# Kernel optimization log

Hardware: AMD Instinct MI355X
Metric: run time of the kernel (lower is better)

Reference implementation:

```python
import jax, jax.numpy as jnp
import numpy as np

B, L, E, D = 4, 1024, 128, 256
NPOI, EPOI, NH, FF = 10000, 128, 8, 256
HD = D // NH


def layer_norm(x, g, b, eps=1e-5):
    m = x.mean(-1, keepdims=True)
    v = ((x - m) ** 2).mean(-1, keepdims=True)
    return (x - m) / jnp.sqrt(v + eps) * g + b


def leaky_relu(x):
    return jnp.where(x >= 0, x, 0.01 * x)


def tokenize_timestamp(t):
    # t: (..., 2) = [timestamp_sec, delta_sec] -> (..., 4) = [week, hour, minute, d_minute]
    week = t[..., 0] % 604800.0 / 86400.0
    hour = t[..., 0] % 86400.0 / 3600.0
    minute = t[..., 0] % 3600.0 / 60.0
    return jnp.stack([week, hour, minute, t[..., 1] / 60.0], -1)


def pos_encode(pos, d):
    # standard sinusoidal PE evaluated at integer positions `pos`
    freq = jnp.exp(-jnp.log(10000.0) * (2.0 * jnp.arange(d // 2, dtype=jnp.float32)) / d)
    ang = pos[..., None].astype(jnp.float32) * freq  # (..., d/2)
    pe = jnp.zeros(pos.shape + (d,), jnp.float32)
    return pe.at[..., 0::2].set(jnp.sin(ang)).at[..., 1::2].set(jnp.cos(ang))


def setup_inputs():
    ks = iter(jax.random.split(jax.random.key(0), 48))

    def nrm(shape, s=0.02):
        return jax.random.normal(next(ks), shape, jnp.float32) * s

    spatial = jax.random.normal(next(ks), (B, L, 2), jnp.float32) * 10.0
    ts = jax.random.uniform(next(ks), (B, L), jnp.float32, 0.0, 1e6)
    dt = jax.random.uniform(next(ks), (B, L), jnp.float32, 0.0, 3600.0)
    token = jax.random.randint(next(ks), (B, L, 2), 0, 2).astype(jnp.float32)
    iq = jnp.zeros((B, L, 4, 2), jnp.float32)
    iq = iq.at[..., 0, 0].set(spatial[..., 0]).at[..., 1, 0].set(spatial[..., 1])
    iq = iq.at[..., 2, 0].set(ts).at[..., 3, 0].set(dt)
    iq = iq.at[..., 0, 1].set(token[..., 0]).at[..., 2, 1].set(token[..., 1])
    positions = jax.random.randint(next(ks), (B, L, 2), 0, L)
    return dict(
        input_seq=iq, positions=positions,
        poi_coors=jax.random.normal(next(ks), (NPOI, 2), jnp.float32) * 10.0,
        poi_embed_mat=nrm((NPOI, EPOI), 1.0),
        sp_w1=nrm((2, E)), sp_b1=jnp.zeros((E,), jnp.float32),
        sp_w2=nrm((E, D)), sp_b2=jnp.zeros((D,), jnp.float32),
        four_w=nrm((4, E), 1.0), four_b=nrm((4, E), 1.0),
        te_w=nrm((4 * E, D)), te_b=jnp.zeros((D,), jnp.float32),
        poi_ln_g=jnp.ones((EPOI,), jnp.float32), poi_ln_b=jnp.zeros((EPOI,), jnp.float32),
        poi_w=nrm((EPOI, D)), poi_b=jnp.zeros((D,), jnp.float32),
        tok_emb=nrm((6, E), 1.0).at[5].set(0.0),
        tok_ln_g=jnp.ones((E,), jnp.float32), tok_ln_b=jnp.zeros((E,), jnp.float32),
        tok_w=nrm((E, D)), tok_b=jnp.zeros((D,), jnp.float32),
        mha_in_w=nrm((D, 3 * D)), mha_in_b=jnp.zeros((3 * D,), jnp.float32),
        mha_out_w=nrm((D, D)), mha_out_b=jnp.zeros((D,), jnp.float32),
        ln1_g=jnp.ones((D,), jnp.float32), ln1_b=jnp.zeros((D,), jnp.float32),
        ff_w1=nrm((D, FF)), ff_b1=jnp.zeros((FF,), jnp.float32),
        ff_w2=nrm((FF, D)), ff_b2=jnp.zeros((D,), jnp.float32),
        ln2_g=jnp.ones((D,), jnp.float32), ln2_b=jnp.zeros((D,), jnp.float32))


def reference(input_seq, positions, poi_coors, poi_embed_mat,
              sp_w1, sp_b1, sp_w2, sp_b2, four_w, four_b, te_w, te_b,
              poi_ln_g, poi_ln_b, poi_w, poi_b,
              tok_emb, tok_ln_g, tok_ln_b, tok_w, tok_b,
              mha_in_w, mha_in_b, mha_out_w, mha_out_b,
              ln1_g, ln1_b, ff_w1, ff_b1, ff_w2, ff_b2, ln2_g, ln2_b):
    token = input_seq[..., jnp.array([0, 2]), 1].astype(jnp.int32)  # (B,L,2)
    spatial = input_seq[:, :, 0:2, 0]                                # (B,L,2)
    tt = tokenize_timestamp(input_seq[:, :, 2:4, 0])                 # (B,L,4)
    # token embedding: Embedding(6) -> LN -> Linear -> (B,L,2,D)
    tok_e = layer_norm(tok_emb[token], tok_ln_g, tok_ln_b) @ tok_w + tok_b
    # spatial embedding (note: original's masked_fill is non-inplace and discarded)
    sp_e = leaky_relu(spatial @ sp_w1 + sp_b1) @ sp_w2 + sp_b2 + tok_e[:, :, 0]
    # brute-force nearest POI: cdist^2 + argmin + gather
    d2 = ((poi_coors[None, None] - spatial[:, :, None]) ** 2).sum(-1)  # (B,L,NPOI)
    poi = jnp.argmin(d2, -1)                                           # (B,L)
    poi_e = layer_norm(poi_embed_mat[poi], poi_ln_g, poi_ln_b) @ poi_w + poi_b + tok_e[:, :, 0]
    # temporal: 4 FourierEncode modules -> concat -> LeakyReLU -> Linear
    t_e = jnp.cos(tt[..., None] * four_w + four_b).reshape(B, L, 4 * E)
    t_e = leaky_relu(t_e) @ te_w + te_b + tok_e[:, :, 1]
    # modal mixer: 1-layer post-norm TransformerEncoder over the 3 modalities
    x = jnp.stack([sp_e, t_e, poi_e], 2).reshape(B * L, 3, D)
    qkv = x @ mha_in_w + mha_in_b
    q, k, v = jnp.split(qkv, 3, -1)
    q = q.reshape(B * L, 3, NH, HD)
    k = k.reshape(B * L, 3, NH, HD)
    v = v.reshape(B * L, 3, NH, HD)
    att = jax.nn.softmax(jnp.einsum('nqhd,nkhd->nhqk', q, k) / jnp.sqrt(jnp.float32(HD)), -1)
    o = jnp.einsum('nhqk,nkhd->nqhd', att, v).reshape(B * L, 3, D) @ mha_out_w + mha_out_b
    x = layer_norm(x + o, ln1_g, ln1_b)
    x = layer_norm(x + (jax.nn.relu(x @ ff_w1 + ff_b1) @ ff_w2 + ff_b2), ln2_g, ln2_b)
    modal_h = x.reshape(B, L, 3, D).mean(2)
    modal_h = modal_h + pos_encode(positions[..., 0], D) + pos_encode(positions[..., 1], D)
    return modal_h  # == mem_seq in the original forward
```

## Files before the change

kernel.cpp:

```cpp
#include <hip/hip_runtime.h>
#include <math.h>

namespace {
constexpr int E = 128, D = 256;
constexpr int NPOI = 10000, NH = 8, FFD = 256;
constexpr int HD = D / NH;
constexpr int NTOK = 4096;
constexpr int TA = 8;
constexpr int TB = 4;
constexpr float LN_EPS = 1e-5f;

constexpr int PK_QKV = 0;
constexpr int PK_OUT = 196608;
constexpr int PK_FF1 = 262144;
constexpr int PK_FF2 = 327680;
constexpr int PK_E0  = 393216;
constexpr int PK_E1  = 458752;
constexpr int PK_E2  = 622592;
constexpr int PK_TOTAL = 688128;
constexpr int NTILES = PK_TOTAL / 512;
}

using frag8 = __attribute__((ext_vector_type(8))) short;
using f32x4 = __attribute__((ext_vector_type(4))) float;

__device__ __forceinline__ float bf2f(short s) {
    union { unsigned u; float f; } x; x.u = ((unsigned)(unsigned short)s) << 16; return x.f;
}
__device__ __forceinline__ unsigned short f2bf(float f) {
    union { float f; unsigned u; } x; x.f = f;
    unsigned r = x.u + 0x7fffu + ((x.u >> 16) & 1u);
    return (unsigned short)(r >> 16);
}

__device__ __forceinline__ float wsum64(float v) {
#pragma unroll
    for (int m = 1; m < 64; m <<= 1) v += __shfl_xor(v, m);
    return v;
}

__device__ __forceinline__ void ln128_bf(const float* __restrict__ src,
                                         const float* __restrict__ g,
                                         const float* __restrict__ b,
                                         short* __restrict__ dst1,
                                         short* __restrict__ dst2, int lane) {
    float v0 = src[lane], v1 = src[64 + lane];
    float mean = wsum64(v0 + v1) * (1.0f / 128.0f);
    float d0 = v0 - mean, d1 = v1 - mean;
    float var = wsum64(d0 * d0 + d1 * d1) * (1.0f / 128.0f);
    float inv = sqrtf(var + LN_EPS);
    float y0 = d0 / inv * g[lane] + b[lane];
    float y1 = d1 / inv * g[64 + lane] + b[64 + lane];
    unsigned short s0 = f2bf(y0), s1 = f2bf(y1);
    dst1[lane] = (short)s0; dst1[64 + lane] = (short)s1;
    if (dst2) { dst2[lane] = (short)s0; dst2[64 + lane] = (short)s1; }
}

__global__ __launch_bounds__(256)
void pack_weights(const float* __restrict__ wqkv, const float* __restrict__ wout,
                  const float* __restrict__ fw1,  const float* __restrict__ fw2,
                  const float* __restrict__ sp_w2, const float* __restrict__ te_w,
                  const float* __restrict__ poi_w, const float* __restrict__ tok_w,
                  unsigned short* __restrict__ pk)
{
    __shared__ float buf[4][32 * 17];
    const int wv = threadIdx.x >> 6, lane = threadIdx.x & 63;
    const int tile = blockIdx.x * 4 + wv;
    if (tile >= NTILES) return;

    int t = tile, sel, base;
    if (t < 384)              { sel = 0; base = PK_QKV; }
    else if ((t -= 384) < 128){ sel = 1; base = PK_OUT; }
    else if ((t -= 128) < 128){ sel = 2; base = PK_FF1; }
    else if ((t -= 128) < 128){ sel = 3; base = PK_FF2; }
    else if ((t -= 128) < 128){ sel = 4; base = PK_E0; }
    else if ((t -= 128) < 320){ sel = 5; base = PK_E1; }
    else                      { t -= 320; sel = 6; base = PK_E2; }
    const int NKT = (sel == 5) ? 20 : 8;
    const int nt = t / NKT, kt = t % NKT;

    const int k = kt * 32 + (lane >> 1);
    const int n0 = nt * 16 + (lane & 1) * 8;
    const float* row;
    switch (sel) {
        case 0:  row = wqkv + (size_t)k * 768; break;
        case 1:  row = wout + (size_t)k * 256; break;
        case 2:  row = fw1  + (size_t)k * 256; break;
        case 3:  row = fw2  + (size_t)k * 256; break;
        case 4:  row = (k < 128) ? sp_w2 + (size_t)k * 256 : tok_w + (size_t)(k - 128) * 256; break;
        case 5:  row = (k < 512) ? te_w  + (size_t)k * 256 : tok_w + (size_t)(k - 512) * 256; break;
        default: row = (k < 128) ? poi_w + (size_t)k * 256 : tok_w + (size_t)(k - 128) * 256; break;
    }
    float4 v0 = *(const float4*)(row + n0);
    float4 v1 = *(const float4*)(row + n0 + 4);
    float* b = buf[wv];
    const int wb = (lane >> 1) * 17 + (lane & 1) * 8;
    b[wb + 0] = v0.x; b[wb + 1] = v0.y; b[wb + 2] = v0.z; b[wb + 3] = v0.w;
    b[wb + 4] = v1.x; b[wb + 5] = v1.y; b[wb + 6] = v1.z; b[wb + 7] = v1.w;
    __syncthreads();

    const int rb = (lane >> 4) * 8, c = lane & 15;
    frag8 fr;
#pragma unroll
    for (int j = 0; j < 8; ++j) fr[j] = (short)f2bf(b[(rb + j) * 17 + c]);
    *(frag8*)(pk + base + ((size_t)t * 64 + lane) * 8) = fr;
}

__global__ __launch_bounds__(256, 2)
void embed_mfma(const float* __restrict__ iq,
                const float* __restrict__ poi_coors,
                const float* __restrict__ poi_embed,
                const float* __restrict__ sp_w1, const float* __restrict__ sp_b1,
                const float* __restrict__ sp_b2,
                const float* __restrict__ four_w, const float* __restrict__ four_b,
                const float* __restrict__ te_b,
                const float* __restrict__ poi_ln_g, const float* __restrict__ poi_ln_b,
                const float* __restrict__ poi_b,
                const float* __restrict__ tok_emb,
                const float* __restrict__ tok_ln_g, const float* __restrict__ tok_ln_b,
                const float* __restrict__ tok_b,
                const unsigned short* __restrict__ pk,
                unsigned short* __restrict__ xout)
{
    constexpr int P0 = 264, P1 = 648, P2 = 264;
    const int tid = threadIdx.x;
    const int w = tid >> 6, lane = tid & 63;
    const int quad = lane >> 4, l16 = lane & 15;
    const int n0 = blockIdx.x * TA;

    __shared__ __align__(16) short U[12544];
    __shared__ __align__(16) short s_x[TA * 768];
    __shared__ float s_meta[TA][6];
    __shared__ int   s_tok[TA][2];
    __shared__ float s_wd[4][TA];
    __shared__ int   s_wi[4][TA];
    __shared__ int   s_poi[TA];

    short* h0 = U;
    short* h1 = U + 2112;
    short* h2 = U + 7296;

    if (tid < TA) {
        const float* p = iq + (size_t)(n0 + tid) * 8;
        s_meta[tid][0] = p[0];
        s_meta[tid][1] = p[2];
        float ts = p[4];
        float dt = p[6];
        s_tok[tid][0] = (int)p[1];
        s_tok[tid][1] = (int)p[5];
        s_meta[tid][2] = fmodf(ts, 604800.0f) / 86400.0f;
        s_meta[tid][3] = fmodf(ts, 86400.0f) / 3600.0f;
        s_meta[tid][4] = fmodf(ts, 3600.0f) / 60.0f;
        s_meta[tid][5] = dt / 60.0f;
    }
    __syncthreads();

    {
        float sx[TA], sy[TA], bd[TA];
        int bi[TA];
#pragma unroll
        for (int t = 0; t < TA; ++t) {
            sx[t] = s_meta[t][0]; sy[t] = s_meta[t][1];
            bd[t] = INFINITY; bi[t] = NPOI;
        }
        const float2* pc = (const float2*)poi_coors;
        for (int i = tid; i < NPOI; i += 256) {
            float2 p = pc[i];
#pragma unroll
            for (int t = 0; t < TA; ++t) {
                float dx = __fsub_rn(p.x, sx[t]);
                float dy = __fsub_rn(p.y, sy[t]);
                float d  = __fadd_rn(__fmul_rn(dx, dx), __fmul_rn(dy, dy));
                if (d < bd[t]) { bd[t] = d; bi[t] = i; }
            }
        }
#pragma unroll
        for (int m = 1; m < 64; m <<= 1) {
#pragma unroll
            for (int t = 0; t < TA; ++t) {
                float od = __shfl_xor(bd[t], m);
                int   oi = __shfl_xor(bi[t], m);
                if (od < bd[t] || (od == bd[t] && oi < bi[t])) { bd[t] = od; bi[t] = oi; }
            }
        }
        if (lane == 0) {
#pragma unroll
            for (int t = 0; t < TA; ++t) { s_wd[w][t] = bd[t]; s_wi[w][t] = bi[t]; }
        }
        __syncthreads();
        if (tid < TA) {
            float bdd = s_wd[0][tid]; int bii = s_wi[0][tid];
#pragma unroll
            for (int ww = 1; ww < 4; ++ww) {
                float od = s_wd[ww][tid]; int oi = s_wi[ww][tid];
                if (od < bdd || (od == bdd && oi < bii)) { bdd = od; bii = oi; }
            }
            s_poi[tid] = bii;
        }
        __syncthreads();
    }

#pragma unroll
    for (int k2 = 0; k2 < 2; ++k2) {
        const int t = w + k2 * 4;
        ln128_bf(tok_emb + (size_t)s_tok[t][0] * E, tok_ln_g, tok_ln_b,
                 h0 + t * P0 + 128, h2 + t * P2 + 128, lane);
        ln128_bf(tok_emb + (size_t)s_tok[t][1] * E, tok_ln_g, tok_ln_b,
                 h1 + t * P1 + 512, nullptr, lane);
        ln128_bf(poi_embed + (size_t)s_poi[t] * E, poi_ln_g, poi_ln_b,
                 h2 + t * P2, nullptr, lane);
    }

    for (int idx = tid; idx < TA * 128; idx += 256) {
        int t = idx >> 7, l = idx & 127;
        float h = s_meta[t][0] * sp_w1[l] + s_meta[t][1] * sp_w1[128 + l] + sp_b1[l];
        h0[t * P0 + l] = (short)f2bf((h >= 0.0f) ? h : 0.01f * h);
    }
    for (int idx = tid; idx < TA * 512; idx += 256) {
        int t = idx >> 9, jj = idx & 511, f = jj >> 7;
        float c = cosf(s_meta[t][2 + f] * four_w[jj] + four_b[jj]);
        h1[t * P1 + jj] = (short)f2bf((c >= 0.0f) ? c : 0.01f * c);
    }
    __syncthreads();

    {
        f32x4 acc[4];
#pragma unroll
        for (int nt = 0; nt < 4; ++nt) {
            int c = w * 64 + nt * 16 + l16;
            float bv = sp_b2[c] + tok_b[c];
            acc[nt][0] = bv; acc[nt][1] = bv; acc[nt][2] = bv; acc[nt][3] = bv;
        }
        for (int kt = 0; kt < 8; ++kt) {
            frag8 a = *(const frag8*)(&h0[l16 * P0 + kt * 32 + quad * 8]);
#pragma unroll
            for (int nt = 0; nt < 4; ++nt) {
                frag8 b = *(const frag8*)(pk + PK_E0 + (((size_t)(w * 4 + nt) * 8 + kt) * 64 + lane) * 8);
                acc[nt] = __builtin_amdgcn_mfma_f32_16x16x32_bf16(a, b, acc[nt], 0, 0, 0);
            }
        }
        if (quad < 2) {
#pragma unroll
            for (int nt = 0; nt < 4; ++nt)
#pragma unroll
                for (int r = 0; r < 4; ++r)
                    s_x[(quad * 4 + r) * 768 + w * 64 + nt * 16 + l16] = (short)f2bf(acc[nt][r]);
        }
    }
    {
        f32x4 acc[4];
#pragma unroll
        for (int nt = 0; nt < 4; ++nt) {
            int c = w * 64 + nt * 16 + l16;
            float bv = te_b[c] + tok_b[c];
            acc[nt][0] = bv; acc[nt][1] = bv; acc[nt][2] = bv; acc[nt][3] = bv;
        }
        for (int kt = 0; kt < 20; ++kt) {
            frag8 a = *(const frag8*)(&h1[l16 * P1 + kt * 32 + quad * 8]);
#pragma unroll
            for (int nt = 0; nt < 4; ++nt) {
                frag8 b = *(const frag8*)(pk + PK_E1 + (((size_t)(w * 4 + nt) * 20 + kt) * 64 + lane) * 8);
                acc[nt] = __builtin_amdgcn_mfma_f32_16x16x32_bf16(a, b, acc[nt], 0, 0, 0);
            }
        }
        if (quad < 2) {
#pragma unroll
            for (int nt = 0; nt < 4; ++nt)
#pragma unroll
                for (int r = 0; r < 4; ++r)
                    s_x[(quad * 4 + r) * 768 + 256 + w * 64 + nt * 16 + l16] = (short)f2bf(acc[nt][r]);
        }
    }
    {
        f32x4 acc[4];
#pragma unroll
        for (int nt = 0; nt < 4; ++nt) {
            int c = w * 64 + nt * 16 + l16;
            float bv = poi_b[c] + tok_b[c];
            acc[nt][0] = bv; acc[nt][1] = bv; acc[nt][2] = bv; acc[nt][3] = bv;
        }
        for (int kt = 0; kt < 8; ++kt) {
            frag8 a = *(const frag8*)(&h2[l16 * P2 + kt * 32 + quad * 8]);
#pragma unroll
            for (int nt = 0; nt < 4; ++nt) {
                frag8 b = *(const frag8*)(pk + PK_E2 + (((size_t)(w * 4 + nt) * 8 + kt) * 64 + lane) * 8);
                acc[nt] = __builtin_amdgcn_mfma_f32_16x16x32_bf16(a, b, acc[nt], 0, 0, 0);
            }
        }
        if (quad < 2) {
#pragma unroll
            for (int nt = 0; nt < 4; ++nt)
#pragma unroll
                for (int r = 0; r < 4; ++r)
                    s_x[(quad * 4 + r) * 768 + 512 + w * 64 + nt * 16 + l16] = (short)f2bf(acc[nt][r]);
        }
    }
    __syncthreads();

    {
        unsigned short* xg = xout + (size_t)n0 * 768;
        for (int c = tid; c < TA * 96; c += 256)
            *(frag8*)(xg + c * 8) = *(const frag8*)(&s_x[c * 8]);
    }
}

__global__ __launch_bounds__(256, 3)
void mha_ff_mfma(const unsigned short* __restrict__ xin,
                 const unsigned short* __restrict__ pk,
                 const float* __restrict__ bqkv, const float* __restrict__ bout,
                 const float* __restrict__ ln1g, const float* __restrict__ ln1b,
                 const float* __restrict__ fb1,  const float* __restrict__ fb2,
                 const float* __restrict__ ln2g, const float* __restrict__ ln2b,
                 const int* __restrict__ positions,
                 float* __restrict__ out)
{
    constexpr int PA = 264;
    constexpr int PQ = 776;
    constexpr int PF = 260;
    const int tid = threadIdx.x;
    const int w = tid >> 6, lane = tid & 63;
    const int quad = lane >> 4, l16 = lane & 15;
    const int n0tok = blockIdx.x * TB;
    const unsigned short* xg = xin + (size_t)n0tok * 3 * D;

    __shared__ __align__(16) short s_a[16 * PA];
    __shared__ __align__(16) char  Uq[25088];
    __shared__ float s_att[TB * NH * 9];

    short* qkv = (short*)Uq;
    float* s_f = (float*)Uq;
    short* s_h = (short*)(Uq + 16640);

    for (int i = tid; i < 12 * 32; i += 256) {
        int row = i >> 5, col = (i & 31) * 8;
        *(frag8*)(&s_a[row * PA + col]) = *(const frag8*)(xg + row * 256 + col);
    }
    __syncthreads();

    float xres[16];

    {
        f32x4 acc[12];
#pragma unroll
        for (int nt = 0; nt < 12; ++nt) {
            float bv = bqkv[w * 192 + nt * 16 + l16];
            acc[nt][0] = bv; acc[nt][1] = bv; acc[nt][2] = bv; acc[nt][3] = bv;
        }
        for (int kt = 0; kt < 8; ++kt) {
            frag8 a = *(const frag8*)(&s_a[l16 * PA + kt * 32 + quad * 8]);
#pragma unroll
            for (int nt = 0; nt < 12; ++nt) {
                frag8 b = *(const frag8*)(pk + PK_QKV + (((size_t)(w * 12 + nt) * 8 + kt) * 64 + lane) * 8);
                acc[nt] = __builtin_amdgcn_mfma_f32_16x16x32_bf16(a, b, acc[nt], 0, 0, 0);
            }
        }
#pragma unroll
        for (int nt = 0; nt < 4; ++nt)
#pragma unroll
            for (int r = 0; r < 4; ++r)
                xres[nt * 4 + r] = bf2f(s_a[(quad * 4 + r) * PA + w * 64 + nt * 16 + l16]);
#pragma unroll
        for (int nt = 0; nt < 12; ++nt)
#pragma unroll
            for (int r = 0; r < 4; ++r) {
                int row = quad * 4 + r, col = w * 192 + nt * 16 + l16;
                qkv[row * PQ + col] = (short)f2bf(acc[nt][r]);
            }
    }
    __syncthreads();

    for (int idx3 = tid; idx3 < TB * NH * 3; idx3 += 256) {
        int tok = idx3 / 24, rem = idx3 % 24;
        int h = rem / 3, qr = rem % 3;
        const short* qp = qkv + (tok * 3 + qr) * PQ + h * HD;
        const short* k0 = qkv + (tok * 3 + 0) * PQ + D + h * HD;
        const short* k1 = qkv + (tok * 3 + 1) * PQ + D + h * HD;
        const short* k2 = qkv + (tok * 3 + 2) * PQ + D + h * HD;
        float s0 = 0.0f, s1 = 0.0f, s2 = 0.0f;
#pragma unroll
        for (int u = 0; u < HD; ++u) {
            float q = bf2f(qp[u]);
            s0 += q * bf2f(k0[u]);
            s1 += q * bf2f(k1[u]);
            s2 += q * bf2f(k2[u]);
        }
        const float sc = 1.0f / sqrtf((float)HD);
        s0 *= sc; s1 *= sc; s2 *= sc;
        float m = fmaxf(s0, fmaxf(s1, s2));
        float e0 = expf(s0 - m), e1 = expf(s1 - m), e2 = expf(s2 - m);
        float inv = 1.0f / (e0 + e1 + e2);
        s_att[idx3 * 3 + 0] = e0 * inv;
        s_att[idx3 * 3 + 1] = e1 * inv;
        s_att[idx3 * 3 + 2] = e2 * inv;
    }
    __syncthreads();

    {
        const int h = tid >> 5;
#pragma unroll
        for (int tok = 0; tok < TB; ++tok) {
            float v0 = bf2f(qkv[(tok * 3 + 0) * PQ + 2 * D + tid]);
            float v1 = bf2f(qkv[(tok * 3 + 1) * PQ + 2 * D + tid]);
            float v2 = bf2f(qkv[(tok * 3 + 2) * PQ + 2 * D + tid]);
#pragma unroll
            for (int qr = 0; qr < 3; ++qr) {
                const float* a = s_att + tok * 72 + h * 9 + qr * 3;
                s_a[(tok * 3 + qr) * PA + tid] = (short)f2bf(a[0] * v0 + a[1] * v1 + a[2] * v2);
            }
        }
    }
    __syncthreads();

    {
        f32x4 acc[4];
#pragma unroll
        for (int nt = 0; nt < 4; ++nt) {
            float bv = bout[w * 64 + nt * 16 + l16];
            acc[nt][0] = bv; acc[nt][1] = bv; acc[nt][2] = bv; acc[nt][3] = bv;
        }
        for (int kt = 0; kt < 8; ++kt) {
            frag8 a = *(const frag8*)(&s_a[l16 * PA + kt * 32 + quad * 8]);
#pragma unroll
            for (int nt = 0; nt < 4; ++nt) {
                frag8 b = *(const frag8*)(pk + PK_OUT + (((size_t)(w * 4 + nt) * 8 + kt) * 64 + lane) * 8);
                acc[nt] = __builtin_amdgcn_mfma_f32_16x16x32_bf16(a, b, acc[nt], 0, 0, 0);
            }
        }
        __syncthreads();
#pragma unroll
        for (int nt = 0; nt < 4; ++nt)
#pragma unroll
            for (int r = 0; r < 4; ++r) {
                int row = quad * 4 + r, col = w * 64 + nt * 16 + l16;
                s_f[row * PF + col] = acc[nt][r] + xres[nt * 4 + r];
            }
    }
    __syncthreads();

#pragma unroll
    for (int rr = 0; rr < 4; ++rr) {
        int row = w + rr * 4, col = lane * 4;
        float4 v = *(const float4*)(&s_f[row * PF + col]);
        float mean = wsum64(v.x + v.y + v.z + v.w) * (1.0f / 256.0f);
        float dx = v.x - mean, dy = v.y - mean, dz = v.z - mean, dw = v.w - mean;
        float var = wsum64(dx * dx + dy * dy + dz * dz + dw * dw) * (1.0f / 256.0f);
        float s = sqrtf(var + LN_EPS);
        float4 g = *(const float4*)(ln1g + col), b = *(const float4*)(ln1b + col);
        float y0 = dx / s * g.x + b.x, y1 = dy / s * g.y + b.y;
        float y2 = dz / s * g.z + b.z, y3 = dw / s * g.w + b.w;
        float4 yv; yv.x = y0; yv.y = y1; yv.z = y2; yv.w = y3;
        *(float4*)(&s_f[row * PF + col]) = yv;
        ushort4 bb; bb.x = f2bf(y0); bb.y = f2bf(y1); bb.z = f2bf(y2); bb.w = f2bf(y3);
        *(ushort4*)(&s_a[row * PA + col]) = bb;
    }
    __syncthreads();

    {
        f32x4 acc[4];
#pragma unroll
        for (int nt = 0; nt < 4; ++nt) {
            float bv = fb1[w * 64 + nt * 16 + l16];
            acc[nt][0] = bv; acc[nt][1] = bv; acc[nt][2] = bv; acc[nt][3] = bv;
        }
        for (int kt = 0; kt < 8; ++kt) {
            frag8 a = *(const frag8*)(&s_a[l16 * PA + kt * 32 + quad * 8]);
#pragma unroll
            for (int nt = 0; nt < 4; ++nt) {
                frag8 b = *(const frag8*)(pk + PK_FF1 + (((size_t)(w * 4 + nt) * 8 + kt) * 64 + lane) * 8);
                acc[nt] = __builtin_amdgcn_mfma_f32_16x16x32_bf16(a, b, acc[nt], 0, 0, 0);
            }
        }
#pragma unroll
        for (int nt = 0; nt < 4; ++nt)
#pragma unroll
            for (int r = 0; r < 4; ++r) {
                int row = quad * 4 + r, col = w * 64 + nt * 16 + l16;
                s_h[row * PA + col] = (short)f2bf(fmaxf(acc[nt][r], 0.0f));
            }
    }
    __syncthreads();

    {
        f32x4 acc[4];
#pragma unroll
        for (int nt = 0; nt < 4; ++nt) {
            float bv = fb2[w * 64 + nt * 16 + l16];
            acc[nt][0] = bv; acc[nt][1] = bv; acc[nt][2] = bv; acc[nt][3] = bv;
        }
        for (int kt = 0; kt < 8; ++kt) {
            frag8 a = *(const frag8*)(&s_h[l16 * PA + kt * 32 + quad * 8]);
#pragma unroll
            for (int nt = 0; nt < 4; ++nt) {
                frag8 b = *(const frag8*)(pk + PK_FF2 + (((size_t)(w * 4 + nt) * 8 + kt) * 64 + lane) * 8);
                acc[nt] = __builtin_amdgcn_mfma_f32_16x16x32_bf16(a, b, acc[nt], 0, 0, 0);
            }
        }
#pragma unroll
        for (int nt = 0; nt < 4; ++nt)
#pragma unroll
            for (int r = 0; r < 4; ++r) {
                int row = quad * 4 + r, col = w * 64 + nt * 16 + l16;
                float y = s_f[row * PF + col];
                s_f[row * PF + col] = acc[nt][r] + y;
            }
    }
    __syncthreads();

#pragma unroll
    for (int rr = 0; rr < 4; ++rr) {
        int row = w + rr * 4, col = lane * 4;
        float4 v = *(const float4*)(&s_f[row * PF + col]);
        float mean = wsum64(v.x + v.y + v.z + v.w) * (1.0f / 256.0f);
        float dx = v.x - mean, dy = v.y - mean, dz = v.z - mean, dw = v.w - mean;
        float var = wsum64(dx * dx + dy * dy + dz * dz + dw * dw) * (1.0f / 256.0f);
        float s = sqrtf(var + LN_EPS);
        float4 g = *(const float4*)(ln2g + col), b = *(const float4*)(ln2b + col);
        float4 zv;
        zv.x = dx / s * g.x + b.x; zv.y = dy / s * g.y + b.y;
        zv.z = dz / s * g.z + b.z; zv.w = dw / s * g.w + b.w;
        *(float4*)(&s_f[row * PF + col]) = zv;
    }
    __syncthreads();

    {
        const int fi = tid >> 1;
        const float freq = expf(-logf(10000.0f) * (2.0f * fi) / (float)D);
#pragma unroll
        for (int t = 0; t < TB; ++t) {
            int n = n0tok + t;
            float m3 = (s_f[(3 * t) * PF + tid] + s_f[(3 * t + 1) * PF + tid] +
                        s_f[(3 * t + 2) * PF + tid]) / 3.0f;
            float p0 = (float)positions[2 * n], p1 = (float)positions[2 * n + 1];
            float a0 = p0 * freq, a1 = p1 * freq;
            float pe = (tid & 1) ? (cosf(a0) + cosf(a1)) : (sinf(a0) + sinf(a1));
            out[(size_t)n * D + tid] = m3 + pe;
        }
    }
}

extern "C" void kernel_launch(void* const* d_in, const int* in_sizes, int n_in,
                              void* d_out, int out_size, void* d_ws, size_t ws_size,
                              hipStream_t stream)
{
    const float* iq        = (const float*)d_in[0];
    const int*   positions = (const int*)d_in[1];
    const float* poi_coors = (const float*)d_in[2];
    const float* poi_embed = (const float*)d_in[3];
    const float* sp_w1     = (const float*)d_in[4];
    const float* sp_b1     = (const float*)d_in[5];
    const float* sp_w2     = (const float*)d_in[6];
    const float* sp_b2     = (const float*)d_in[7];
    const float* four_w    = (const float*)d_in[8];
    const float* four_b    = (const float*)d_in[9];
    const float* te_w      = (const float*)d_in[10];
    const float* te_b      = (const float*)d_in[11];
    const float* poi_ln_g  = (const float*)d_in[12];
    const float* poi_ln_b  = (const float*)d_in[13];
    const float* poi_w     = (const float*)d_in[14];
    const float* poi_b     = (const float*)d_in[15];
    const float* tok_emb   = (const float*)d_in[16];
    const float* tok_ln_g  = (const float*)d_in[17];
    const float* tok_ln_b  = (const float*)d_in[18];
    const float* tok_w     = (const float*)d_in[19];
    const float* tok_b     = (const float*)d_in[20];
    const float* mha_in_w  = (const float*)d_in[21];
    const float* mha_in_b  = (const float*)d_in[22];
    const float* mha_out_w = (const float*)d_in[23];
    const float* mha_out_b = (const float*)d_in[24];
    const float* ln1_g     = (const float*)d_in[25];
    const float* ln1_b     = (const float*)d_in[26];
    const float* ff_w1     = (const float*)d_in[27];
    const float* ff_b1     = (const float*)d_in[28];
    const float* ff_w2     = (const float*)d_in[29];
    const float* ff_b2     = (const float*)d_in[30];
    const float* ln2_g     = (const float*)d_in[31];
    const float* ln2_b     = (const float*)d_in[32];

    unsigned short* pkw = (unsigned short*)d_ws;
    unsigned short* xws = (unsigned short*)((char*)d_ws + PK_TOTAL * 2);

    pack_weights<<<NTILES / 4, 256, 0, stream>>>(
        mha_in_w, mha_out_w, ff_w1, ff_w2, sp_w2, te_w, poi_w, tok_w, pkw);

    embed_mfma<<<NTOK / TA, 256, 0, stream>>>(
        iq, poi_coors, poi_embed, sp_w1, sp_b1, sp_b2, four_w, four_b, te_b,
        poi_ln_g, poi_ln_b, poi_b, tok_emb, tok_ln_g, tok_ln_b, tok_b,
        pkw, xws);

    mha_ff_mfma<<<NTOK / TB, 256, 0, stream>>>(
        xws, pkw, mha_in_b, mha_out_b, ln1_g, ln1_b,
        ff_b1, ff_b2, ln2_g, ln2_b, positions, (float*)d_out);
}
```

Before: 204.8 us.

## Process eight tokens per block in MHA/FF kernel to reuse weight fragments

Doubles the tokens handled per block in the fused MHA+FFN kernel from 4 to 8, giving 24 rows, which are computed as two 16-row MFMA tiles sharing each loaded weight fragment. This halves global weight traffic per token and halves the block count. In exchange it uses more registers and LDS, lowers the launch-bounds occupancy hint from 3 to 2, and leaves 8 of the 32 MFMA rows as padding. The remaining unshown sections (attention loop, positional encoding, output) must also handle TB=8 correctly.

```diff
diff --git a/kernel.cpp b/kernel.cpp
--- a/kernel.cpp
+++ b/kernel.cpp
@@ -7,7 +7,7 @@
 constexpr int HD = D / NH;
 constexpr int NTOK = 4096;
 constexpr int TA = 8;
-constexpr int TB = 4;
+constexpr int TB = 8;
 constexpr float LN_EPS = 1e-5f;
 
 constexpr int PK_QKV = 0;
@@ -304,7 +304,7 @@
     }
 }
 
-__global__ __launch_bounds__(256, 3)
+__global__ __launch_bounds__(256, 2)
 void mha_ff_mfma(const unsigned short* __restrict__ xin,
                  const unsigned short* __restrict__ pk,
                  const float* __restrict__ bqkv, const float* __restrict__ bout,
@@ -317,54 +317,68 @@
     constexpr int PA = 264;
     constexpr int PQ = 776;
     constexpr int PF = 260;
+    constexpr int NROW = 3 * TB;
     const int tid = threadIdx.x;
     const int w = tid >> 6, lane = tid & 63;
     const int quad = lane >> 4, l16 = lane & 15;
     const int n0tok = blockIdx.x * TB;
     const unsigned short* xg = xin + (size_t)n0tok * 3 * D;
 
-    __shared__ __align__(16) short s_a[16 * PA];
-    __shared__ __align__(16) char  Uq[25088];
+    __shared__ __align__(16) short s_a[32 * PA];
+    __shared__ __align__(16) char  Uq[41856];
     __shared__ float s_att[TB * NH * 9];
 
     short* qkv = (short*)Uq;
     float* s_f = (float*)Uq;
-    short* s_h = (short*)(Uq + 16640);
-
-    for (int i = tid; i < 12 * 32; i += 256) {
+    short* s_h = (short*)(Uq + 24960);
+
+    for (int i = tid; i < NROW * 32; i += 256) {
         int row = i >> 5, col = (i & 31) * 8;
         *(frag8*)(&s_a[row * PA + col]) = *(const frag8*)(xg + row * 256 + col);
     }
     __syncthreads();
 
-    float xres[16];
-
-    {
-        f32x4 acc[12];
+    float xres[32];
+
+    {
+        f32x4 acc[24];
 #pragma unroll
         for (int nt = 0; nt < 12; ++nt) {
             float bv = bqkv[w * 192 + nt * 16 + l16];
-            acc[nt][0] = bv; acc[nt][1] = bv; acc[nt][2] = bv; acc[nt][3] = bv;
+#pragma unroll
+            for (int m = 0; m < 2; ++m) {
+                acc[nt * 2 + m][0] = bv; acc[nt * 2 + m][1] = bv;
+                acc[nt * 2 + m][2] = bv; acc[nt * 2 + m][3] = bv;
+            }
         }
         for (int kt = 0; kt < 8; ++kt) {
-            frag8 a = *(const frag8*)(&s_a[l16 * PA + kt * 32 + quad * 8]);
+            frag8 a0 = *(const frag8*)(&s_a[l16 * PA + kt * 32 + quad * 8]);
+            frag8 a1 = *(const frag8*)(&s_a[(16 + l16) * PA + kt * 32 + quad * 8]);
 #pragma unroll
             for (int nt = 0; nt < 12; ++nt) {
                 frag8 b = *(const frag8*)(pk + PK_QKV + (((size_t)(w * 12 + nt) * 8 + kt) * 64 + lane) * 8);
-                acc[nt] = __builtin_amdgcn_mfma_f32_16x16x32_bf16(a, b, acc[nt], 0, 0, 0);
-            }
-        }
-#pragma unroll
-        for (int nt = 0; nt < 4; ++nt)
-#pragma unroll
-            for (int r = 0; r < 4; ++r)
-                xres[nt * 4 + r] = bf2f(s_a[(quad * 4 + r) * PA + w * 64 + nt * 16 + l16]);
+                acc[nt * 2 + 0] = __builtin_amdgcn_mfma_f32_16x16x32_bf16(a0, b, acc[nt * 2 + 0], 0, 0, 0);
+                acc[nt * 2 + 1] = __builtin_amdgcn_mfma_f32_16x16x32_bf16(a1, b, acc[nt * 2 + 1], 0, 0, 0);
+            }
+        }
+#pragma unroll
+        for (int m = 0; m < 2; ++m)
+#pragma unroll
+            for (int nt = 0; nt < 4; ++nt)
+#pragma unroll
+                for (int r = 0; r < 4; ++r)
+                    xres[m * 16 + nt * 4 + r] =
+                        bf2f(s_a[(m * 16 + quad * 4 + r) * PA + w * 64 + nt * 16 + l16]);
 #pragma unroll
         for (int nt = 0; nt < 12; ++nt)
 #pragma unroll
-            for (int r = 0; r < 4; ++r) {
-                int row = quad * 4 + r, col = w * 192 + nt * 16 + l16;
-                qkv[row * PQ + col] = (short)f2bf(acc[nt][r]);
+            for (int m = 0; m < 2; ++m) {
+                if (m == 1 && quad >= 2) continue;
+#pragma unroll
+                for (int r = 0; r < 4; ++r) {
+                    int row = m * 16 + quad * 4 + r, col = w * 192 + nt * 16 + l16;
+                    qkv[row * PQ + col] = (short)f2bf(acc[nt * 2 + m][r]);
+                }
             }
     }
     __syncthreads();
@@ -412,33 +426,43 @@
     __syncthreads();
 
     {
-        f32x4 acc[4];
+        f32x4 acc[8];
 #pragma unroll
         for (int nt = 0; nt < 4; ++nt) {
             float bv = bout[w * 64 + nt * 16 + l16];
-            acc[nt][0] = bv; acc[nt][1] = bv; acc[nt][2] = bv; acc[nt][3] = bv;
+#pragma unroll
+            for (int m = 0; m < 2; ++m) {
+                acc[nt * 2 + m][0] = bv; acc[nt * 2 + m][1] = bv;
+                acc[nt * 2 + m][2] = bv; acc[nt * 2 + m][3] = bv;
+            }
         }
         for (int kt = 0; kt < 8; ++kt) {
-            frag8 a = *(const frag8*)(&s_a[l16 * PA + kt * 32 + quad * 8]);
+            frag8 a0 = *(const frag8*)(&s_a[l16 * PA + kt * 32 + quad * 8]);
+            frag8 a1 = *(const frag8*)(&s_a[(16 + l16) * PA + kt * 32 + quad * 8]);
 #pragma unroll
             for (int nt = 0; nt < 4; ++nt) {
                 frag8 b = *(const frag8*)(pk + PK_OUT + (((size_t)(w * 4 + nt) * 8 + kt) * 64 + lane) * 8);
-                acc[nt] = __builtin_amdgcn_mfma_f32_16x16x32_bf16(a, b, acc[nt], 0, 0, 0);
+                acc[nt * 2 + 0] = __builtin_amdgcn_mfma_f32_16x16x32_bf16(a0, b, acc[nt * 2 + 0], 0, 0, 0);
+                acc[nt * 2 + 1] = __builtin_amdgcn_mfma_f32_16x16x32_bf16(a1, b, acc[nt * 2 + 1], 0, 0, 0);
             }
         }
         __syncthreads();
 #pragma unroll
-        for (int nt = 0; nt < 4; ++nt)
-#pragma unroll
-            for (int r = 0; r < 4; ++r) {
-                int row = quad * 4 + r, col = w * 64 + nt * 16 + l16;
-                s_f[row * PF + col] = acc[nt][r] + xres[nt * 4 + r];
-            }
-    }
-    __syncthreads();
-
-#pragma unroll
-    for (int rr = 0; rr < 4; ++rr) {
+        for (int m = 0; m < 2; ++m) {
+            if (m == 1 && quad >= 2) continue;
+#pragma unroll
+            for (int nt = 0; nt < 4; ++nt)
+#pragma unroll
+                for (int r = 0; r < 4; ++r) {
+                    int row = m * 16 + quad * 4 + r, col = w * 64 + nt * 16 + l16;
+                    s_f[row * PF + col] = acc[nt * 2 + m][r] + xres[m * 16 + nt * 4 + r];
+                }
+        }
+    }
+    __syncthreads();
+
+#pragma unroll
+    for (int rr = 0; rr < 6; ++rr) {
         int row = w + rr * 4, col = lane * 4;
         float4 v = *(const float4*)(&s_f[row * PF + col]);
         float mean = wsum64(v.x + v.y + v.z + v.w) * (1.0f / 256.0f);
@@ -456,58 +480,78 @@
     __syncthreads();
 
     {
-        f32x4 acc[4];
+        f32x4 acc[8];
 #pragma unroll
         for (int nt = 0; nt < 4; ++nt) {
             float bv = fb1[w * 64 + nt * 16 + l16];
-            acc[nt][0] = bv; acc[nt][1] = bv; acc[nt][2] = bv; acc[nt][3] = bv;
+#pragma unroll
+            for (int m = 0; m < 2; ++m) {
+                acc[nt * 2 + m][0] = bv; acc[nt * 2 + m][1] = bv;
+                acc[nt * 2 + m][2] = bv; acc[nt * 2 + m][3] = bv;
+            }
         }
         for (int kt = 0; kt < 8; ++kt) {
-            frag8 a = *(const frag8*)(&s_a[l16 * PA + kt * 32 + quad * 8]);
+            frag8 a0 = *(const frag8*)(&s_a[l16 * PA + kt * 32 + quad * 8]);
+            frag8 a1 = *(const frag8*)(&s_a[(16 + l16) * PA + kt * 32 + quad * 8]);
 #pragma unroll
             for (int nt = 0; nt < 4; ++nt) {
                 frag8 b = *(const frag8*)(pk + PK_FF1 + (((size_t)(w * 4 + nt) * 8 + kt) * 64 + lane) * 8);
-                acc[nt] = __builtin_amdgcn_mfma_f32_16x16x32_bf16(a, b, acc[nt], 0, 0, 0);
-            }
-        }
-#pragma unroll
-        for (int nt = 0; nt < 4; ++nt)
-#pragma unroll
-            for (int r = 0; r < 4; ++r) {
-                int row = quad * 4 + r, col = w * 64 + nt * 16 + l16;
-                s_h[row * PA + col] = (short)f2bf(fmaxf(acc[nt][r], 0.0f));
-            }
-    }
-    __syncthreads();
-
-    {
-        f32x4 acc[4];
+                acc[nt * 2 + 0] = __builtin_amdgcn_mfma_f32_16x16x32_bf16(a0, b, acc[nt * 2 + 0], 0, 0, 0);
+                acc[nt * 2 + 1] = __builtin_amdgcn_mfma_f32_16x16x32_bf16(a1, b, acc[nt * 2 + 1], 0, 0, 0);
+            }
+        }
+#pragma unroll
+        for (int m = 0; m < 2; ++m) {
+            if (m == 1 && quad >= 2) continue;
+#pragma unroll
+            for (int nt = 0; nt < 4; ++nt)
+#pragma unroll
+                for (int r = 0; r < 4; ++r) {
+                    int row = m * 16 + quad * 4 + r, col = w * 64 + nt * 16 + l16;
+                    s_h[row * PA + col] = (short)f2bf(fmaxf(acc[nt * 2 + m][r], 0.0f));
+                }
+        }
+    }
+    __syncthreads();
+
+    {
+        f32x4 acc[8];
 #pragma unroll
         for (int nt = 0; nt < 4; ++nt) {
             float bv = fb2[w * 64 + nt * 16 + l16];
-            acc[nt][0] = bv; acc[nt][1] = bv; acc[nt][2] = bv; acc[nt][3] = bv;
+#pragma unroll
+            for (int m = 0; m < 2; ++m) {
+                acc[nt * 2 + m][0] = bv; acc[nt * 2 + m][1] = bv;
+                acc[nt * 2 + m][2] = bv; acc[nt * 2 + m][3] = bv;
+            }
         }
         for (int kt = 0; kt < 8; ++kt) {
-            frag8 a = *(const frag8*)(&s_h[l16 * PA + kt * 32 + quad * 8]);
+            frag8 a0 = *(const frag8*)(&s_h[l16 * PA + kt * 32 + quad * 8]);
+            frag8 a1 = *(const frag8*)(&s_h[(16 + l16) * PA + kt * 32 + quad * 8]);
 #pragma unroll
             for (int nt = 0; nt < 4; ++nt) {
                 frag8 b = *(const frag8*)(pk + PK_FF2 + (((size_t)(w * 4 + nt) * 8 + kt) * 64 + lane) * 8);
-                acc[nt] = __builtin_amdgcn_mfma_f32_16x16x32_bf16(a, b, acc[nt], 0, 0, 0);
-            }
-        }
-#pragma unroll
-        for (int nt = 0; nt < 4; ++nt)
-#pragma unroll
-            for (int r = 0; r < 4; ++r) {
-                int row = quad * 4 + r, col = w * 64 + nt * 16 + l16;
-                float y = s_f[row * PF + col];
-                s_f[row * PF + col] = acc[nt][r] + y;
-            }
-    }
-    __syncthreads();
-
-#pragma unroll
-    for (int rr = 0; rr < 4; ++rr) {
+                acc[nt * 2 + 0] = __builtin_amdgcn_mfma_f32_16x16x32_bf16(a0, b, acc[nt * 2 + 0], 0, 0, 0);
+                acc[nt * 2 + 1] = __builtin_amdgcn_mfma_f32_16x16x32_bf16(a1, b, acc[nt * 2 + 1], 0, 0, 0);
+            }
+        }
+#pragma unroll
+        for (int m = 0; m < 2; ++m) {
+            if (m == 1 && quad >= 2) continue;
+#pragma unroll
+            for (int nt = 0; nt < 4; ++nt)
+#pragma unroll
+                for (int r = 0; r < 4; ++r) {
+                    int row = m * 16 + quad * 4 + r, col = w * 64 + nt * 16 + l16;
+                    float y = s_f[row * PF + col];
+                    s_f[row * PF + col] = acc[nt * 2 + m][r] + y;
+                }
+        }
+    }
+    __syncthreads();
+
+#pragma unroll
+    for (int rr = 0; rr < 6; ++rr) {
         int row = w + rr * 4, col = lane * 4;
         float4 v = *(const float4*)(&s_f[row * PF + col]);
         float mean = wsum64(v.x + v.y + v.z + v.w) * (1.0f / 256.0f);
```

Result: no change. 207.6 us (+1.3%).
